# Performance work log

Hardware: AMD Instinct MI355X
Metric: run time of the kernel (lower is better)

## Reference

```python
import jax, jax.numpy as jnp
import numpy as np

H = 512  # GRU hidden size

def _conv(x, w, b, stride):
    y = jax.lax.conv_general_dilated(x, w, (stride, stride), 'VALID',
                                     dimension_numbers=('NCHW', 'OIHW', 'NCHW'))
    return jax.nn.relu(y + b[None, :, None, None])

def setup_inputs() -> dict:
    key = jax.random.key(0)
    ks = jax.random.split(key, 20)
    T, N, C, HW, A = 32, 16, 4, 124, 6
    TN = T * N
    s = 0.05
    return {
        'inputs': jax.random.uniform(ks[0], (TN, C, HW, HW), jnp.float32),
        'states': jax.random.normal(ks[1], (N, H), jnp.float32),
        'masks': jnp.ones((TN, 1), jnp.float32),
        'action': jax.random.randint(ks[2], (TN,), 0, A, jnp.int64),
        'conv1_w': jax.random.normal(ks[3], (32, C, 8, 8), jnp.float32) * s,
        'conv1_b': jnp.zeros((32,), jnp.float32),
        'conv2_w': jax.random.normal(ks[4], (64, 32, 4, 4), jnp.float32) * s,
        'conv2_b': jnp.zeros((64,), jnp.float32),
        'conv3_w': jax.random.normal(ks[5], (32, 64, 3, 3), jnp.float32) * s,
        'conv3_b': jnp.zeros((32,), jnp.float32),
        'fc_w': jax.random.normal(ks[6], (H, 32 * 12 * 12), jnp.float32) * 0.02,
        'fc_b': jnp.zeros((H,), jnp.float32),
        'w_ih': jax.random.normal(ks[7], (3 * H, H), jnp.float32) * 0.04,
        'w_hh': jax.random.normal(ks[8], (3 * H, H), jnp.float32) * 0.04,
        'b_ih': jnp.zeros((3 * H,), jnp.float32),
        'b_hh': jnp.zeros((3 * H,), jnp.float32),
        'actor_w': jax.random.normal(ks[9], (A, H), jnp.float32) * 0.04,
        'actor_b': jnp.zeros((A,), jnp.float32),
        'critic_w': jax.random.normal(ks[10], (1, H), jnp.float32) * 0.04,
        'critic_b': jnp.zeros((1,), jnp.float32),
    }

def reference(inputs, states, masks, action,
              conv1_w, conv1_b, conv2_w, conv2_b, conv3_w, conv3_b,
              fc_w, fc_b, w_ih, w_hh, b_ih, b_hh,
              actor_w, actor_b, critic_w, critic_b):
    # CNN trunk (inputs scaled by 1/255 as in the original)
    x = inputs * (1.0 / 255.0)
    x = _conv(x, conv1_w, conv1_b, 4)
    x = _conv(x, conv2_w, conv2_b, 2)
    x = _conv(x, conv3_w, conv3_b, 1)
    x = x.reshape(x.shape[0], -1)                      # [TN, 32*12*12]
    x = jax.nn.relu(x @ fc_w.T + fc_b)                 # [TN, H]

    N = states.shape[0]
    T = x.shape[0] // N
    xs = x.reshape(T, N, H)
    ms = masks.reshape(T, N, 1)
    # input-to-hidden GEMM hoisted out of the recurrence
    gi = jnp.einsum('tnh,gh->tng', xs, w_ih) + b_ih    # [T, N, 3H]

    def step(h, xm):
        g_i, m = xm
        h = h * m                                      # mask-reset folded into step
        gh = h @ w_hh.T + b_hh
        r = jax.nn.sigmoid(g_i[:, :H] + gh[:, :H])
        z = jax.nn.sigmoid(g_i[:, H:2 * H] + gh[:, H:2 * H])
        n = jnp.tanh(g_i[:, 2 * H:] + r * gh[:, 2 * H:])
        h_new = (1.0 - z) * n + z * h
        return h_new, h_new

    states_out, outs = jax.lax.scan(step, states, (gi, ms))
    x = outs.reshape(T * N, H)

    logits = x @ actor_w.T + actor_b
    logp = jax.nn.log_softmax(logits, axis=-1)
    action_log_probs = jnp.take_along_axis(logp, action[:, None], axis=1)[:, 0]
    entropy = -jnp.sum(jnp.exp(logp) * logp, axis=-1)
    value = x @ critic_w.T + critic_b
    return value, action_log_probs, entropy, states_out
```

## Files before the change

### kernel.cpp

```cpp
#include <hip/hip_runtime.h>
#include <hip/hip_bf16.h>


typedef __bf16 bf16x8_t __attribute__((ext_vector_type(8)));
typedef float  f32x4_t  __attribute__((ext_vector_type(4)));

__device__ __forceinline__ unsigned int pack_bf2(float a, float b) {
  union { __bf16 h[2]; unsigned int u; } c;
  c.h[0] = (__bf16)a; c.h[1] = (__bf16)b;
  return c.u;
}
__device__ __forceinline__ unsigned short f2bf(float x) {
  union { __bf16 h; unsigned short s; } c; c.h = (__bf16)x; return c.s;
}

__global__ __launch_bounds__(256, 2) void conv1_mfma(const float* __restrict__ x,
        const float* __restrict__ w, const float* __restrict__ bias,
        unsigned short* __restrict__ out) {
  __shared__ __align__(16) unsigned short img[4*64*140];
  const int tid  = threadIdx.x;
  const int lane = tid & 63;
  const int wv   = tid >> 6;
  const int n    = blockIdx.x >> 1;
  const int half = blockIdx.x & 1;
  const int y0   = half * 60;
  {
    #pragma unroll
    for (int it = 0; it < 31; ++it) {
      int i  = it*256 + tid;
      int c  = i / 1984;
      int r  = i - c*1984;
      int y  = r / 31;
      int xq = r - y*31;
      const float4 f = *(const float4*)(x + ((size_t)(n*4 + c)*124 + (y0 + y))*124 + xq*4);
      uint2 v; v.x = pack_bf2(f.x, f.y); v.y = pack_bf2(f.z, f.w);
      *(uint2*)&img[(c*64 + y)*140 + xq*4] = v;
    }
  }
  bf16x8_t wfr[2][8];
  {
    int m = lane & 15, q = lane >> 4;
    #pragma unroll
    for (int tt = 0; tt < 2; ++tt) {
      const float* wrow = w + (size_t)(tt*16 + m)*256 + q*8;
      #pragma unroll
      for (int ks = 0; ks < 8; ++ks) {
        float4 f0 = *(const float4*)(wrow + ks*32);
        float4 f1 = *(const float4*)(wrow + ks*32 + 4);
        bf16x8_t v;
        v[0]=(__bf16)f0.x; v[1]=(__bf16)f0.y; v[2]=(__bf16)f0.z; v[3]=(__bf16)f0.w;
        v[4]=(__bf16)f1.x; v[5]=(__bf16)f1.y; v[6]=(__bf16)f1.z; v[7]=(__bf16)f1.w;
        wfr[tt][ks] = v;
      }
    }
  }
  __syncthreads();
  const int m = lane & 15, q = lane >> 4;
  int rb[8];
  #pragma unroll
  for (int ks = 0; ks < 8; ++ks) {
    int kk = ks*32 + q*8;
    rb[ks] = (kk >> 6)*64 + ((kk >> 3) & 7);
  }
  const float sc = 1.0f / 255.0f;
  for (int tile = wv; tile < 29; tile += 4) {
    int pl = tile*16 + m;
    int ok = pl < 450;
    if (!ok) pl = 449;
    int t = pl / 30, opx = pl - t*30;
    int t4 = t*4, opx4 = opx*4;
    f32x4_t acc0 = {0.f,0.f,0.f,0.f}, acc1 = {0.f,0.f,0.f,0.f};
    #pragma unroll
    for (int ks = 0; ks < 8; ++ks) {
      const unsigned short* p = &img[(rb[ks] + t4)*140 + opx4];
      union { bf16x8_t v; uint2 u[2]; } fb;
      fb.u[0] = *(const uint2*)p;
      fb.u[1] = *(const uint2*)(p + 4);
      acc0 = __builtin_amdgcn_mfma_f32_16x16x32_bf16(wfr[0][ks], fb.v, acc0, 0, 0, 0);
      acc1 = __builtin_amdgcn_mfma_f32_16x16x32_bf16(wfr[1][ks], fb.v, acc1, 0, 0, 0);
    }
    if (ok) {
      int opy = half*15 + t;
      size_t obase = (size_t)n*32*900 + opy*30 + opx;
      #pragma unroll
      for (int rg = 0; rg < 4; ++rg) {
        int oc0 = q*4 + rg;
        out[obase + (size_t)oc0*900]      = f2bf(fmaxf(acc0[rg]*sc + bias[oc0], 0.f));
        out[obase + (size_t)(oc0+16)*900] = f2bf(fmaxf(acc1[rg]*sc + bias[oc0+16], 0.f));
      }
    }
  }
}

__global__ __launch_bounds__(256, 2) void conv2_mfma(const unsigned short* __restrict__ in,
        const float* __restrict__ w, const float* __restrict__ bias,
        unsigned short* __restrict__ out) {
  __shared__ __align__(16) unsigned short img[28800];
  const int tid  = threadIdx.x;
  const int lane = tid & 63;
  const int wv   = tid >> 6;
  const int n    = blockIdx.x;
  {
    const uint4* src = (const uint4*)(in + (size_t)n*28800);
    uint4* dst = (uint4*)img;
    #pragma unroll
    for (int j = 0; j < 15; ++j) {
      int s = j*256 + tid;
      if (s < 3600) dst[s] = src[s];
    }
  }
  bf16x8_t wfr[16];
  {
    int m = lane & 15, q = lane >> 4;
    const float* wrow = w + (size_t)(wv*16 + m)*512 + q*8;
    #pragma unroll
    for (int ks = 0; ks < 16; ++ks) {
      float4 f0 = *(const float4*)(wrow + ks*32);
      float4 f1 = *(const float4*)(wrow + ks*32 + 4);
      bf16x8_t v;
      v[0] = (__bf16)f0.x; v[1] = (__bf16)f0.y; v[2] = (__bf16)f0.z; v[3] = (__bf16)f0.w;
      v[4] = (__bf16)f1.x; v[5] = (__bf16)f1.y; v[6] = (__bf16)f1.z; v[7] = (__bf16)f1.w;
      wfr[ks] = v;
    }
  }
  __syncthreads();
  const int m  = lane & 15;
  const int qq = lane >> 4;
  const int cl  = qq >> 1;
  const int ky0 = (qq & 1) * 2;
  float b4[4];
  #pragma unroll
  for (int rg = 0; rg < 4; ++rg) b4[rg] = bias[wv*16 + qq*4 + rg];
  for (int tile = 0; tile < 13; ++tile) {
    int px = tile*16 + m;
    int valid = px < 196;
    int pc = valid ? px : 195;
    int oy = pc / 14, ox = pc % 14;
    const unsigned short* pb = &img[((cl*30) + oy*2 + ky0)*30 + ox*2];
    f32x4_t acc = {0.f, 0.f, 0.f, 0.f};
    #pragma unroll
    for (int ks = 0; ks < 16; ++ks) {
      const unsigned short* p0 = pb + ks*1800;
      union { bf16x8_t v; unsigned int u[4]; } fb;
      fb.u[0] = *(const unsigned int*)(p0);
      fb.u[1] = *(const unsigned int*)(p0 + 2);
      fb.u[2] = *(const unsigned int*)(p0 + 30);
      fb.u[3] = *(const unsigned int*)(p0 + 32);
      acc = __builtin_amdgcn_mfma_f32_16x16x32_bf16(wfr[ks], fb.v, acc, 0, 0, 0);
    }
    if (valid) {
      #pragma unroll
      for (int rg = 0; rg < 4; ++rg) {
        int oc = wv*16 + qq*4 + rg;
        out[((size_t)n*64 + oc)*196 + px] = f2bf(fmaxf(acc[rg] + b4[rg], 0.f));
      }
    }
  }
}

__global__ __launch_bounds__(256) void conv3_mfma(const unsigned short* __restrict__ in,
        const float* __restrict__ w, const float* __restrict__ bias,
        unsigned short* __restrict__ out) {
  __shared__ __align__(16) unsigned short img[196*72];
  const int tid  = threadIdx.x;
  const int lane = tid & 63;
  const int wv   = tid >> 6;
  const int n    = blockIdx.x;
  {
    const unsigned short* src = in + (size_t)n*12544;
    for (int i = tid; i < 3136; i += 256) {
      int c = i / 49, j = i - c*49;
      uint2 v = *(const uint2*)(src + c*196 + j*4);
      int px = j*4;
      img[(px+0)*72 + c] = (unsigned short)(v.x);
      img[(px+1)*72 + c] = (unsigned short)(v.x >> 16);
      img[(px+2)*72 + c] = (unsigned short)(v.y);
      img[(px+3)*72 + c] = (unsigned short)(v.y >> 16);
    }
  }
  bf16x8_t wfr[2][18];
  {
    int m = lane & 15, q = lane >> 4;
    #pragma unroll
    for (int tt = 0; tt < 2; ++tt) {
      const float* wrow = w + (size_t)(tt*16 + m)*576;
      #pragma unroll
      for (int ks = 0; ks < 18; ++ks) {
        int g = ks >> 1;
        int c0 = (ks & 1)*32 + q*8;
        bf16x8_t v;
        #pragma unroll
        for (int e = 0; e < 8; ++e) v[e] = (__bf16)wrow[(c0 + e)*9 + g];
        wfr[tt][ks] = v;
      }
    }
  }
  __syncthreads();
  const int m = lane & 15, q = lane >> 4;
  for (int tile = wv; tile < 9; tile += 4) {
    int px = tile*16 + m;
    int oy = px / 12, ox = px % 12;
    f32x4_t a0 = {0.f,0.f,0.f,0.f}, a1 = {0.f,0.f,0.f,0.f};
    #pragma unroll
    for (int ks = 0; ks < 18; ++ks) {
      int g = ks >> 1, ky = g / 3, kx = g % 3;
      int c0 = (ks & 1)*32 + q*8;
      const unsigned short* p = &img[((oy + ky)*14 + ox + kx)*72 + c0];
      union { bf16x8_t v; uint4 u; } fb;
      fb.u = *(const uint4*)p;
      a0 = __builtin_amdgcn_mfma_f32_16x16x32_bf16(wfr[0][ks], fb.v, a0, 0, 0, 0);
      a1 = __builtin_amdgcn_mfma_f32_16x16x32_bf16(wfr[1][ks], fb.v, a1, 0, 0, 0);
    }
    #pragma unroll
    for (int rg = 0; rg < 4; ++rg) {
      int oc = q*4 + rg;
      out[((size_t)n*32 + oc)*144 + px]      = f2bf(fmaxf(a0[rg] + bias[oc], 0.f));
      out[((size_t)n*32 + oc + 16)*144 + px] = f2bf(fmaxf(a1[rg] + bias[oc + 16], 0.f));
    }
  }
}

__global__ __launch_bounds__(256) void cvt_w_k(const float* __restrict__ w,
        unsigned short* __restrict__ o) {
  int i = (blockIdx.x*256 + threadIdx.x) * 8;
  float4 f0 = *(const float4*)(w + i);
  float4 f1 = *(const float4*)(w + i + 4);
  uint4 v;
  v.x = pack_bf2(f0.x, f0.y); v.y = pack_bf2(f0.z, f0.w);
  v.z = pack_bf2(f1.x, f1.y); v.w = pack_bf2(f1.z, f1.w);
  *(uint4*)(o + i) = v;
}

__global__ __launch_bounds__(256) void fc_mfma(const unsigned short* __restrict__ A,
        const unsigned short* __restrict__ Wb, float* __restrict__ part) {
  __shared__ __align__(16) unsigned short As[64*72];
  __shared__ __align__(16) unsigned short Wsm[64*72];
  const int tid  = threadIdx.x;
  const int lane = tid & 63;
  const int wv   = tid >> 6;
  const int m0 = blockIdx.y * 64, n0 = blockIdx.x * 64;
  const int kz = blockIdx.z * 1152;
  const int r  = tid >> 2;
  const int cq = (tid & 3) * 16;
  f32x4_t acc[4] = {{0,0,0,0},{0,0,0,0},{0,0,0,0},{0,0,0,0}};
  for (int k0 = 0; k0 < 1152; k0 += 64) {
    __syncthreads();
    {
      const uint4* src = (const uint4*)(A + (size_t)(m0 + r)*4608 + kz + k0 + cq);
      uint4 a0 = src[0], a1 = src[1];
      *(uint4*)&As[r*72 + cq]     = a0;
      *(uint4*)&As[r*72 + cq + 8] = a1;
    }
    {
      const uint4* src = (const uint4*)(Wb + (size_t)(n0 + r)*4608 + kz + k0 + cq);
      uint4 w0 = src[0], w1 = src[1];
      *(uint4*)&Wsm[r*72 + cq]     = w0;
      *(uint4*)&Wsm[r*72 + cq + 8] = w1;
    }
    __syncthreads();
    #pragma unroll
    for (int kk = 0; kk < 2; ++kk) {
      union { bf16x8_t v; uint4 u; } bf;
      bf.u = *(const uint4*)&As[(wv*16 + (lane & 15))*72 + kk*32 + (lane >> 4)*8];
      #pragma unroll
      for (int tt = 0; tt < 4; ++tt) {
        union { bf16x8_t v; uint4 u; } af;
        af.u = *(const uint4*)&Wsm[(tt*16 + (lane & 15))*72 + kk*32 + (lane >> 4)*8];
        acc[tt] = __builtin_amdgcn_mfma_f32_16x16x32_bf16(af.v, bf.v, acc[tt], 0, 0, 0);
      }
    }
  }
  {
    int m = m0 + wv*16 + (lane & 15);
    int q4 = lane >> 4;
    float* dst = part + (size_t)blockIdx.z*262144;
    #pragma unroll
    for (int tt = 0; tt < 4; ++tt) {
      #pragma unroll
      for (int rg = 0; rg < 4; ++rg) {
        int n = n0 + tt*16 + q4*4 + rg;
        dst[(size_t)m*512 + n] = acc[tt][rg];
      }
    }
  }
}

__global__ __launch_bounds__(256) void fc_red(const float* __restrict__ part,
        const float* __restrict__ bias, float* __restrict__ C) {
  int idx = blockIdx.x*256 + threadIdx.x;
  int nq = idx & 127;
  const float4* p = (const float4*)part;
  float4 s0 = p[idx];
  float4 s1 = p[65536 + idx];
  float4 s2 = p[131072 + idx];
  float4 s3 = p[196608 + idx];
  float4 b = *(const float4*)(bias + nq*4);
  float4 r;
  r.x = fmaxf(s0.x + s1.x + s2.x + s3.x + b.x, 0.f);
  r.y = fmaxf(s0.y + s1.y + s2.y + s3.y + b.y, 0.f);
  r.z = fmaxf(s0.z + s1.z + s2.z + s3.z + b.z, 0.f);
  r.w = fmaxf(s0.w + s1.w + s2.w + s3.w + b.w, 0.f);
  ((float4*)C)[idx] = r;
}

__global__ __launch_bounds__(256) void gi_mfma(const float* __restrict__ A,
        const float* __restrict__ W, const float* __restrict__ bias,
        float* __restrict__ C) {
  __shared__ __align__(16) unsigned short Ash[64*72], Asl[64*72];
  __shared__ __align__(16) unsigned short Wsh[64*72], Wsl[64*72];
  const int tid  = threadIdx.x;
  const int lane = tid & 63;
  const int wv   = tid >> 6;
  const int m0 = blockIdx.y * 64, n0 = blockIdx.x * 64;
  const int r  = tid >> 2;
  const int cq = (tid & 3) * 16;
  f32x4_t acc[4] = {{0,0,0,0},{0,0,0,0},{0,0,0,0},{0,0,0,0}};
  for (int k0 = 0; k0 < 512; k0 += 64) {
    __syncthreads();
    #pragma unroll
    for (int op = 0; op < 2; ++op) {
      const float* src = (op ? W + (size_t)(n0 + r)*512 : A + (size_t)(m0 + r)*512) + k0 + cq;
      unsigned short* dh = (op ? Wsh : Ash) + r*72 + cq;
      unsigned short* dl = (op ? Wsl : Asl) + r*72 + cq;
      #pragma unroll
      for (int hb = 0; hb < 2; ++hb) {
        float4 f0 = *(const float4*)(src + hb*8);
        float4 f1 = *(const float4*)(src + hb*8 + 4);
        float v[8] = {f0.x,f0.y,f0.z,f0.w,f1.x,f1.y,f1.z,f1.w};
        uint4 vh, vl;
        unsigned int* ph = (unsigned int*)&vh;
        unsigned int* pl = (unsigned int*)&vl;
        #pragma unroll
        for (int e = 0; e < 4; ++e) {
          float a = v[e*2], b = v[e*2+1];
          __bf16 ah = (__bf16)a, bh = (__bf16)b;
          union { __bf16 h[2]; unsigned int u; } ch, clo;
          ch.h[0] = ah; ch.h[1] = bh;
          clo.h[0] = (__bf16)(a - (float)ah); clo.h[1] = (__bf16)(b - (float)bh);
          ph[e] = ch.u; pl[e] = clo.u;
        }
        *(uint4*)(dh + hb*8) = vh;
        *(uint4*)(dl + hb*8) = vl;
      }
    }
    __syncthreads();
    #pragma unroll
    for (int kk = 0; kk < 2; ++kk) {
      int boff = (wv*16 + (lane & 15))*72 + kk*32 + (lane >> 4)*8;
      union { bf16x8_t v; uint4 u; } bh, bl;
      bh.u = *(const uint4*)&Ash[boff];
      bl.u = *(const uint4*)&Asl[boff];
      #pragma unroll
      for (int tt = 0; tt < 4; ++tt) {
        int aoff = (tt*16 + (lane & 15))*72 + kk*32 + (lane >> 4)*8;
        union { bf16x8_t v; uint4 u; } ah, al;
        ah.u = *(const uint4*)&Wsh[aoff];
        al.u = *(const uint4*)&Wsl[aoff];
        acc[tt] = __builtin_amdgcn_mfma_f32_16x16x32_bf16(ah.v, bh.v, acc[tt], 0, 0, 0);
        acc[tt] = __builtin_amdgcn_mfma_f32_16x16x32_bf16(ah.v, bl.v, acc[tt], 0, 0, 0);
        acc[tt] = __builtin_amdgcn_mfma_f32_16x16x32_bf16(al.v, bh.v, acc[tt], 0, 0, 0);
      }
    }
  }
  {
    int m = m0 + wv*16 + (lane & 15);
    int q4 = lane >> 4;
    #pragma unroll
    for (int tt = 0; tt < 4; ++tt) {
      #pragma unroll
      for (int rg = 0; rg < 4; ++rg) {
        int n = n0 + tt*16 + q4*4 + rg;
        C[(size_t)m*1536 + n] = acc[tt][rg] + bias[n];
      }
    }
  }
}

#define GRU_NB 8
__global__ __launch_bounds__(512) void gru_k(const float* __restrict__ gi, const float* __restrict__ states,
    const float* __restrict__ masks, const float* __restrict__ w_hh, const float* __restrict__ b_hh,
    float* __restrict__ outs, unsigned int* __restrict__ hbuf, int* __restrict__ flags,
    float* __restrict__ states_out) {
  __shared__ __align__(16) unsigned short hbf[16*520];
  __shared__ float hp_s[16*64];
  __shared__ float gh_s[192*17];
  __shared__ float bhs[192];
  __shared__ float mask_s[512];
  const int b    = blockIdx.x;
  const int tid  = threadIdx.x;
  const int lane = tid & 63;
  const int wv   = tid >> 6;
  const int jbase = b * 64;
  const int gn = tid >> 5;
  const int gj = (tid & 31) * 2;

  mask_s[tid < 512 ? tid : 0] = masks[tid < 512 ? tid : 0];
  if (tid < 192) bhs[tid] = b_hh[(tid >> 6)*512 + jbase + (tid & 63)];

  bf16x8_t wfr[2][16];
  {
    int r = lane & 15, q = lane >> 4;
    #pragma unroll
    for (int ti = 0; ti < 2; ++ti) {
      int tt = wv + ti*8;
      if (tt < 12) {
        int g = tt >> 2, jt = (tt & 3) * 16;
        const float* wrow = w_hh + (size_t)(g*512 + jbase + jt + r)*512 + q*8;
        #pragma unroll
        for (int ks = 0; ks < 16; ++ks) {
          float4 f0 = *(const float4*)(wrow + ks*32);
          float4 f1 = *(const float4*)(wrow + ks*32 + 4);
          bf16x8_t v;
          v[0] = (__bf16)f0.x; v[1] = (__bf16)f0.y; v[2] = (__bf16)f0.z; v[3] = (__bf16)f0.w;
          v[4] = (__bf16)f1.x; v[5] = (__bf16)f1.y; v[6] = (__bf16)f1.z; v[7] = (__bf16)f1.w;
          wfr[ti][ks] = v;
        }
      }
    }
  }
  __syncthreads();

  for (int t = 0; t < 32; ++t) {
    const float* gip = gi + (size_t)(t*16 + gn)*1536 + jbase + gj;
    float2 giR = *(const float2*)(gip);
    float2 giZ = *(const float2*)(gip + 512);
    float2 giN = *(const float2*)(gip + 1024);

    if (t == 0) {
      for (int i = tid; i < 4096; i += 512) {
        int nn = i >> 8, kp = (i & 255) * 2;
        float m = mask_s[nn];
        float f0 = states[nn*512 + kp], f1 = states[nn*512 + kp + 1];
        *(unsigned int*)&hbf[nn*520 + kp] = pack_bf2(f0*m, f1*m);
      }
      {
        float m0 = mask_s[gn];
        hp_s[gn*64 + gj]     = states[gn*512 + jbase + gj] * m0;
        hp_s[gn*64 + gj + 1] = states[gn*512 + jbase + gj + 1] * m0;
      }
      __syncthreads();
    } else {
      {
        int done = 0;
        while (!done) {
          int ok = 1;
          if (lane < 8) {
            int v = __hip_atomic_load(&flags[lane*16], __ATOMIC_RELAXED, __HIP_MEMORY_SCOPE_AGENT);
            ok = (v >= t);
          }
          done = __all(ok);
          if (!done) __builtin_amdgcn_s_sleep(1);
        }
      }
      {
        const unsigned long long* hsrc =
            (const unsigned long long*)(hbuf + (t & 1)*4096);
        #pragma unroll
        for (int idx = tid; idx < 1792; idx += 512) {
          int s  = idx >> 8;
          int p  = s + (s >= b);
          int rem = idx & 255;
          int nn = rem >> 4;
          int jw = rem & 15;
          unsigned long long u = __hip_atomic_load(hsrc + p*256 + nn*16 + jw,
                                 __ATOMIC_RELAXED, __HIP_MEMORY_SCOPE_AGENT);
          *(unsigned long long*)&hbf[nn*520 + p*64 + jw*4] = u;
        }
      }
      __syncthreads();
    }

    {
      int r = lane & 15, q = lane >> 4;
      const unsigned short* hrow = &hbf[r*520 + q*8];
      #pragma unroll
      for (int ti = 0; ti < 2; ++ti) {
        int tt = wv + ti*8;
        if (tt < 12) {
          f32x4_t acc = {0.f, 0.f, 0.f, 0.f};
          #pragma unroll
          for (int ks = 0; ks < 16; ++ks) {
            union { bf16x8_t v; uint4 u; } fb;
            fb.u = *(const uint4*)(hrow + ks*32);
            acc = __builtin_amdgcn_mfma_f32_16x16x32_bf16(wfr[ti][ks], fb.v, acc, 0, 0, 0);
          }
          int g = tt >> 2, jt = (tt & 3) * 16;
          #pragma unroll
          for (int rg = 0; rg < 4; ++rg)
            gh_s[(g*64 + jt + q*4 + rg)*17 + r] = acc[rg];
        }
      }
    }
    __syncthreads();

    {
      float ghr0 = gh_s[(gj    )*17 + gn] + bhs[gj];
      float ghr1 = gh_s[(gj + 1)*17 + gn] + bhs[gj + 1];
      float ghz0 = gh_s[(64 + gj)*17 + gn] + bhs[64 + gj];
      float ghz1 = gh_s[(65 + gj)*17 + gn] + bhs[65 + gj];
      float ghn0 = gh_s[(128 + gj)*17 + gn] + bhs[128 + gj];
      float ghn1 = gh_s[(129 + gj)*17 + gn] + bhs[129 + gj];
      float r0 = 1.f / (1.f + expf(-(giR.x + ghr0)));
      float r1 = 1.f / (1.f + expf(-(giR.y + ghr1)));
      float z0 = 1.f / (1.f + expf(-(giZ.x + ghz0)));
      float z1 = 1.f / (1.f + expf(-(giZ.y + ghz1)));
      float n0 = tanhf(giN.x + r0*ghn0);
      float n1 = tanhf(giN.y + r1*ghn1);
      float hp0 = hp_s[gn*64 + gj];
      float hp1 = hp_s[gn*64 + gj + 1];
      float hn0 = (1.f - z0)*n0 + z0*hp0;
      float hn1 = (1.f - z1)*n1 + z1*hp1;
      float mnext = (t < 31) ? mask_s[(t+1)*16 + gn] : 0.f;
      float hm0 = hn0 * mnext, hm1 = hn1 * mnext;
      if (t < 31) {
        __hip_atomic_store(hbuf + ((t+1)&1)*4096 + b*512 + gn*32 + (gj >> 1),
                           pack_bf2(hm0, hm1), __ATOMIC_RELAXED, __HIP_MEMORY_SCOPE_AGENT);
      }
      __syncthreads();
      if (t < 31) {
        if (tid == 0)
          __hip_atomic_store(&flags[b*16], t + 1, __ATOMIC_RELAXED, __HIP_MEMORY_SCOPE_AGENT);
        *(float2*)&outs[(size_t)(t*16 + gn)*512 + jbase + gj] = make_float2(hn0, hn1);
        hp_s[gn*64 + gj]     = hm0;
        hp_s[gn*64 + gj + 1] = hm1;
        *(unsigned int*)&hbf[gn*520 + jbase + gj] = pack_bf2(hm0, hm1);
      } else {
        *(float2*)&outs[(size_t)(t*16 + gn)*512 + jbase + gj] = make_float2(hn0, hn1);
        *(float2*)&states_out[gn*512 + jbase + gj] = make_float2(hn0, hn1);
      }
    }
  }
}

__global__ __launch_bounds__(256) void heads_k(const float* __restrict__ xs, const int* __restrict__ action,
    const float* __restrict__ aw, const float* __restrict__ ab,
    const float* __restrict__ cw, const float* __restrict__ cb, float* __restrict__ out) {
  int row  = blockIdx.x * 4 + (threadIdx.x >> 6);
  int lane = threadIdx.x & 63;
  const float* xr = xs + (size_t)row * 512;
  float acc[7];
  #pragma unroll
  for (int a = 0; a < 7; ++a) acc[a] = 0.f;
  #pragma unroll
  for (int kb = 0; kb < 8; ++kb) {
    int k = kb*64 + lane;
    float xv = xr[k];
    #pragma unroll
    for (int a = 0; a < 6; ++a) acc[a] += xv * aw[a*512 + k];
    acc[6] += xv * cw[k];
  }
  #pragma unroll
  for (int off = 32; off > 0; off >>= 1) {
    #pragma unroll
    for (int a = 0; a < 7; ++a) acc[a] += __shfl_down(acc[a], off);
  }
  if (lane == 0) {
    float lg[6];
    #pragma unroll
    for (int a = 0; a < 6; ++a) lg[a] = acc[a] + ab[a];
    float mx = lg[0];
    #pragma unroll
    for (int a = 1; a < 6; ++a) mx = fmaxf(mx, lg[a]);
    float se = 0.f;
    #pragma unroll
    for (int a = 0; a < 6; ++a) se += expf(lg[a] - mx);
    float lse = mx + logf(se);
    float ent = 0.f;
    #pragma unroll
    for (int a = 0; a < 6; ++a) { float lp = lg[a] - lse; ent -= expf(lp)*lp; }
    int ai = action[row];
    out[row]        = acc[6] + cb[0];
    out[512  + row] = lg[ai] - lse;
    out[1024 + row] = ent;
  }
}

extern "C" void kernel_launch(void* const* d_in, const int* in_sizes, int n_in,
                              void* d_out, int out_size, void* d_ws, size_t ws_size,
                              hipStream_t stream) {
  const float* x      = (const float*)d_in[0];
  const float* states = (const float*)d_in[1];
  const float* masks  = (const float*)d_in[2];
  const int*   action = (const int*)d_in[3];
  const float* c1w = (const float*)d_in[4];
  const float* c1b = (const float*)d_in[5];
  const float* c2w = (const float*)d_in[6];
  const float* c2b = (const float*)d_in[7];
  const float* c3w = (const float*)d_in[8];
  const float* c3b = (const float*)d_in[9];
  const float* fcw = (const float*)d_in[10];
  const float* fcb = (const float*)d_in[11];
  const float* wih = (const float*)d_in[12];
  const float* whh = (const float*)d_in[13];
  const float* bih = (const float*)d_in[14];
  const float* bhh = (const float*)d_in[15];
  const float* aw  = (const float*)d_in[16];
  const float* ab  = (const float*)d_in[17];
  const float* cw  = (const float*)d_in[18];
  const float* cb  = (const float*)d_in[19];
  (void)in_sizes; (void)n_in; (void)out_size; (void)ws_size;

  float* ws = (float*)d_ws;
  unsigned short* o1b = (unsigned short*)ws;
  unsigned short* o2b = (unsigned short*)(ws + 14745600);
  unsigned short* o3b = (unsigned short*)ws;
  float* xs    = ws + 2359296;
  float* gibuf = ws + 2621440;
  float* outs  = ws + 3407872;
  unsigned int* hbuf = (unsigned int*)(ws + 3670016);
  int*   flags = (int*)(ws + 3686400);
  unsigned short* wbf = (unsigned short*)(ws + 7372800);
  float* fcpart = ws + 8552448;
  float* out   = (float*)d_out;

  cvt_w_k<<<1152, 256, 0, stream>>>(fcw, wbf);
  conv1_mfma<<<1024, 256, 0, stream>>>(x, c1w, c1b, o1b);
  conv2_mfma<<<512, 256, 0, stream>>>(o1b, c2w, c2b, o2b);
  conv3_mfma<<<512, 256, 0, stream>>>(o2b, c3w, c3b, o3b);
  fc_mfma<<<dim3(8, 8, 4), 256, 0, stream>>>(o3b, wbf, fcpart);
  fc_red<<<256, 256, 0, stream>>>(fcpart, fcb, xs);
  gi_mfma<<<dim3(24, 8), 256, 0, stream>>>(xs, wih, bih, gibuf);
  hipMemsetAsync(flags, 0, 1024 * sizeof(int), stream);
  gru_k<<<GRU_NB, 512, 0, stream>>>(gibuf, states, masks, whh, bhh, outs, hbuf, flags, out + 1536);
  heads_k<<<128, 256, 0, stream>>>(outs, action, aw, ab, cw, cb, out);
}
```

Before: 464.1 us.

## Use per-wave flags in GRU recurrence, fast activations, fold flag reset into cvt kernel

The cross-block GRU handshake moves from one flag per block, set after a block-wide barrier, to one flag per wave. Each wave publishes its slice of the hidden state, waits on its own stores and sets its flag, and consumer waves poll only the matching producer waves and copy just that slice. This is meant to shorten the serial critical path of each of the 32 timesteps. Sigmoid and tanh are replaced with __expf plus hardware reciprocal approximations, and the flag memset is folded into the weight conversion kernel to drop one API call, at some cost in accuracy and added complexity in the memory-ordering logic.

```diff
diff --git a/kernel.cpp b/kernel.cpp
--- a/kernel.cpp
+++ b/kernel.cpp
@@ -12,6 +12,13 @@
 }
 __device__ __forceinline__ unsigned short f2bf(float x) {
   union { __bf16 h; unsigned short s; } c; c.h = (__bf16)x; return c.s;
+}
+__device__ __forceinline__ float fsig(float x) {
+  return __builtin_amdgcn_rcpf(1.f + __expf(-x));
+}
+__device__ __forceinline__ float ftanh_f(float x) {
+  float e = __expf(2.f * x);
+  return 1.f - 2.f * __builtin_amdgcn_rcpf(e + 1.f);
 }
 
 __global__ __launch_bounds__(256, 2) void conv1_mfma(const float* __restrict__ x,
@@ -221,7 +228,8 @@
 }
 
 __global__ __launch_bounds__(256) void cvt_w_k(const float* __restrict__ w,
-        unsigned short* __restrict__ o) {
+        unsigned short* __restrict__ o, int* __restrict__ flags) {
+  if (blockIdx.x == 0) ((int4*)flags)[threadIdx.x] = make_int4(0, 0, 0, 0);
   int i = (blockIdx.x*256 + threadIdx.x) * 8;
   float4 f0 = *(const float4*)(w + i);
   float4 f1 = *(const float4*)(w + i + 4);
@@ -444,8 +452,9 @@
         int done = 0;
         while (!done) {
           int ok = 1;
-          if (lane < 8) {
-            int v = __hip_atomic_load(&flags[lane*16], __ATOMIC_RELAXED, __HIP_MEMORY_SCOPE_AGENT);
+          if (lane < 7) {
+            int p = lane + (lane >= b);
+            int v = __hip_atomic_load(&flags[(p*8 + wv)*16], __ATOMIC_RELAXED, __HIP_MEMORY_SCOPE_AGENT);
             ok = (v >= t);
           }
           done = __all(ok);
@@ -453,18 +462,15 @@
         }
       }
       {
-        const unsigned long long* hsrc =
-            (const unsigned long long*)(hbuf + (t & 1)*4096);
+        const unsigned int* hsrc = hbuf + (t & 1)*4096;
+        const int gn2 = 2*wv + (lane >> 5);
+        const int jw  = lane & 31;
         #pragma unroll
-        for (int idx = tid; idx < 1792; idx += 512) {
-          int s  = idx >> 8;
-          int p  = s + (s >= b);
-          int rem = idx & 255;
-          int nn = rem >> 4;
-          int jw = rem & 15;
-          unsigned long long u = __hip_atomic_load(hsrc + p*256 + nn*16 + jw,
-                                 __ATOMIC_RELAXED, __HIP_MEMORY_SCOPE_AGENT);
-          *(unsigned long long*)&hbf[nn*520 + p*64 + jw*4] = u;
+        for (int k = 0; k < 7; ++k) {
+          int p = k + (k >= b);
+          unsigned int u = __hip_atomic_load(hsrc + p*512 + wv*64 + lane,
+                                             __ATOMIC_RELAXED, __HIP_MEMORY_SCOPE_AGENT);
+          *(unsigned int*)&hbf[gn2*520 + p*64 + jw*2] = u;
         }
       }
       __syncthreads();
@@ -500,26 +506,24 @@
       float ghz1 = gh_s[(65 + gj)*17 + gn] + bhs[65 + gj];
       float ghn0 = gh_s[(128 + gj)*17 + gn] + bhs[128 + gj];
       float ghn1 = gh_s[(129 + gj)*17 + gn] + bhs[129 + gj];
-      float r0 = 1.f / (1.f + expf(-(giR.x + ghr0)));
-      float r1 = 1.f / (1.f + expf(-(giR.y + ghr1)));
-      float z0 = 1.f / (1.f + expf(-(giZ.x + ghz0)));
-      float z1 = 1.f / (1.f + expf(-(giZ.y + ghz1)));
-      float n0 = tanhf(giN.x + r0*ghn0);
-      float n1 = tanhf(giN.y + r1*ghn1);
+      float r0 = fsig(giR.x + ghr0);
+      float r1 = fsig(giR.y + ghr1);
+      float z0 = fsig(giZ.x + ghz0);
+      float z1 = fsig(giZ.y + ghz1);
+      float n0 = ftanh_f(giN.x + r0*ghn0);
+      float n1 = ftanh_f(giN.y + r1*ghn1);
       float hp0 = hp_s[gn*64 + gj];
       float hp1 = hp_s[gn*64 + gj + 1];
       float hn0 = (1.f - z0)*n0 + z0*hp0;
       float hn1 = (1.f - z1)*n1 + z1*hp1;
-      float mnext = (t < 31) ? mask_s[(t+1)*16 + gn] : 0.f;
-      float hm0 = hn0 * mnext, hm1 = hn1 * mnext;
       if (t < 31) {
+        float mnext = mask_s[(t+1)*16 + gn];
+        float hm0 = hn0 * mnext, hm1 = hn1 * mnext;
         __hip_atomic_store(hbuf + ((t+1)&1)*4096 + b*512 + gn*32 + (gj >> 1),
                            pack_bf2(hm0, hm1), __ATOMIC_RELAXED, __HIP_MEMORY_SCOPE_AGENT);
-      }
-      __syncthreads();
-      if (t < 31) {
-        if (tid == 0)
-          __hip_atomic_store(&flags[b*16], t + 1, __ATOMIC_RELAXED, __HIP_MEMORY_SCOPE_AGENT);
+        asm volatile("s_waitcnt vmcnt(0)" ::: "memory");
+        if (lane == 0)
+          __hip_atomic_store(&flags[(b*8 + wv)*16], t + 1, __ATOMIC_RELAXED, __HIP_MEMORY_SCOPE_AGENT);
         *(float2*)&outs[(size_t)(t*16 + gn)*512 + jbase + gj] = make_float2(hn0, hn1);
         hp_s[gn*64 + gj]     = hm0;
         hp_s[gn*64 + gj + 1] = hm1;
@@ -613,14 +617,13 @@
   float* fcpart = ws + 8552448;
   float* out   = (float*)d_out;
 
-  cvt_w_k<<<1152, 256, 0, stream>>>(fcw, wbf);
+  cvt_w_k<<<1152, 256, 0, stream>>>(fcw, wbf, flags);
   conv1_mfma<<<1024, 256, 0, stream>>>(x, c1w, c1b, o1b);
   conv2_mfma<<<512, 256, 0, stream>>>(o1b, c2w, c2b, o2b);
   conv3_mfma<<<512, 256, 0, stream>>>(o2b, c3w, c3b, o3b);
   fc_mfma<<<dim3(8, 8, 4), 256, 0, stream>>>(o3b, wbf, fcpart);
   fc_red<<<256, 256, 0, stream>>>(fcpart, fcb, xs);
   gi_mfma<<<dim3(24, 8), 256, 0, stream>>>(xs, wih, bih, gibuf);
-  hipMemsetAsync(flags, 0, 1024 * sizeof(int), stream);
   gru_k<<<GRU_NB, 512, 0, stream>>>(gibuf, states, masks, whh, bhh, outs, hbuf, flags, out + 1536);
   heads_k<<<128, 256, 0, stream>>>(outs, action, aw, ab, cw, cb, out);
 }
```

Measured after the change: 491.0 us. 1.06x slower.
